# Kernel tuning notes

Hardware: AMD Instinct MI355X
Metric: run time of the kernel (lower is better)

Reference implementation:

```python
import jax, jax.numpy as jnp
import numpy as np

N, E, K, D = 100000, 3200000, 1024, 11


def setup_inputs() -> dict:
    key = jax.random.key(0)
    ks = jax.random.split(key, 11)
    return {
        "x": jax.random.normal(ks[0], (N, D), jnp.float32),
        "edge_index": jax.random.randint(ks[1], (2, E), 0, N, dtype=jnp.int32),
        "ready_idx": jnp.sort(jax.random.randint(ks[2], (K,), 0, N, dtype=jnp.int32)),
        "W1": jax.random.normal(ks[3], (D, 64), jnp.float32) * 0.2,
        "b1": jax.random.normal(ks[4], (64,), jnp.float32) * 0.02,
        "W2": jax.random.normal(ks[5], (75, 1), jnp.float32) * 0.2,
        "b2": jax.random.normal(ks[6], (1,), jnp.float32) * 0.02,
        "Wd": jax.random.normal(ks[7], (64, 1), jnp.float32) * 0.2,
        "bd": jax.random.normal(ks[8], (1,), jnp.float32) * 0.02,
        "Wv": jax.random.normal(ks[9], (64, 1), jnp.float32) * 0.2,
        "bv": jax.random.normal(ks[10], (1,), jnp.float32) * 0.02,
    }


def gcn_conv(x, W, b, src, dst):
    """PyG GCNConv with flow='target_to_source': gather from dst, aggregate at src.
    Symmetric normalization with self-loops (weight 1)."""
    n = x.shape[0]
    h = x @ W  # [N, F_out]
    loop = jnp.arange(n, dtype=src.dtype)
    s = jnp.concatenate([src, loop])  # aggregation index (row for target_to_source)
    d = jnp.concatenate([dst, loop])  # gather index
    deg = jax.ops.segment_sum(jnp.ones(s.shape, h.dtype), s, num_segments=n)
    dis = jnp.where(deg > 0, jax.lax.rsqrt(jnp.maximum(deg, 1e-12)), 0.0)
    norm = dis[s] * dis[d]  # [E+N]
    out = jax.ops.segment_sum(norm[:, None] * h[d], s, num_segments=n)
    return out + b


def reference(x, edge_index, ready_idx, W1, b1, W2, b2, Wd, bd, Wv, bv):
    src, dst = edge_index[0], edge_index[1]
    h = jax.nn.relu(gcn_conv(x, W1, b1, src, dst))           # [N, 64]
    x_input = jnp.concatenate([h, x], axis=1)                # [N, 75]
    probs_n = gcn_conv(x_input, W2, b2, src, dst)            # [N, 1]
    x_mean = jnp.mean(h, axis=0)                             # [64]
    v = x_mean @ Wv + bv                                     # [1]
    prob_nothing = x_mean @ Wd + bd                          # [1]
    logits = jnp.concatenate([probs_n[ready_idx, 0], prob_nothing])  # [K+1]
    probs = jax.nn.softmax(logits)
    return probs, v
```

## Files before the change

kernel.cpp:

```cpp
#include <hip/hip_runtime.h>
#include <hip/hip_fp16.h>
#include <math.h>

#define N_ 100000
#define E_ 3200000
#define K_ 1024
#define D_ 11
#define NBUCK_ 391
#define NPAD_ (NBUCK_ * 256)
#define CAPB_ 16384
#define CAP_ 32
#define CAPW_ 33
#define GB_ 512
#define CHUNK_ 6256
#define SA_ 8
#define SD_ 4
#define XC_ 32
#define RSEG_ 4096
#define RSTRIDE_ 16

static inline size_t align512(size_t x) { return (x + 511) & ~(size_t)511; }

__device__ inline float2 h2f(unsigned int u) {
    __half2 h = *reinterpret_cast<__half2*>(&u);
    return __half22float2(h);
}

__global__ void k_prep(const float* __restrict__ x, const int* __restrict__ ready,
                       __half* __restrict__ xh,
                       int* __restrict__ deg, float* __restrict__ pr_raw,
                       unsigned char* __restrict__ flag, float* __restrict__ xpart,
                       int* __restrict__ bcur, int* __restrict__ rcntp) {
    int i = blockIdx.x * blockDim.x + threadIdx.x;
    if (i < N_ * 16) {
        int n = i >> 4, j = i & 15;
        if (j < D_) xh[i] = __float2half_rn(x[n * D_ + j]);
    }
    if (i < N_) {
        deg[i] = 0; pr_raw[i] = 0.f;
        int lo = 0, hi = K_ - 1, f = 0;
        while (lo <= hi) {
            int mid = (lo + hi) >> 1;
            int v = ready[mid];
            if (v == i) { f = 1; break; }
            if (v < i) lo = mid + 1; else hi = mid - 1;
        }
        flag[i] = (unsigned char)f;
    }
    if (i < XC_ * 64) xpart[i] = 0.f;
    if (i < NBUCK_) bcur[i] = i * CAPB_;
    if (i < 32 * RSTRIDE_) rcntp[i] = 0;
}

__global__ __launch_bounds__(256) void k_bin(const int* __restrict__ src,
                                             const int* __restrict__ dst,
                                             int* __restrict__ bcur,
                                             int* __restrict__ gbuf) {
    __shared__ int sbuf[NBUCK_ * CAPW_];
    __shared__ int scnt[NBUCK_];
    int t = threadIdx.x;
    for (int b = t; b < NBUCK_; b += 256) scnt[b] = 0;
    __syncthreads();
    long e0 = (long)blockIdx.x * CHUNK_;
    for (int r = 0; r < CHUNK_; r += 2048) {
        int off = r + t * 8;
        long i0 = e0 + off;
        if (off < CHUNK_ && i0 + 7 < E_) {
            int4 s0 = *(const int4*)(src + i0);
            int4 s1 = *(const int4*)(src + i0 + 4);
            int4 d0 = *(const int4*)(dst + i0);
            int4 d1 = *(const int4*)(dst + i0 + 4);
            int ss[8] = {s0.x, s0.y, s0.z, s0.w, s1.x, s1.y, s1.z, s1.w};
            int dd[8] = {d0.x, d0.y, d0.z, d0.w, d1.x, d1.y, d1.z, d1.w};
#pragma unroll
            for (int q = 0; q < 8; q++) {
                int b = ss[q] >> 8;
                int pack = ((ss[q] & 255) << 17) | dd[q];
                int pos = atomicAdd(&scnt[b], 1);
                if (pos < CAP_) sbuf[b * CAPW_ + pos] = pack;
                else gbuf[atomicAdd(&bcur[b], 1)] = pack;
            }
        }
    }
    __syncthreads();
    for (int b = t; b < NBUCK_; b += 256) {
        int c = min(scnt[b], CAP_);
        while (c >= 16) {
            int g = atomicAdd(&bcur[b], 16);
            c -= 16;
            if ((g & 3) == 0) {
                int4* gp = (int4*)(gbuf + g);
#pragma unroll
                for (int q = 0; q < 4; q++)
                    gp[q] = make_int4(sbuf[b*CAPW_ + c + 4*q],
                                      sbuf[b*CAPW_ + c + 4*q + 1],
                                      sbuf[b*CAPW_ + c + 4*q + 2],
                                      sbuf[b*CAPW_ + c + 4*q + 3]);
            } else {
                for (int k = 0; k < 16; k++) gbuf[g + k] = sbuf[b*CAPW_ + c + k];
            }
        }
        if (c > 0) {
            int g = atomicAdd(&bcur[b], c);
            for (int k = 0; k < c; k++) gbuf[g + k] = sbuf[b*CAPW_ + k];
        }
    }
}

__global__ __launch_bounds__(256) void k_deg(const int* __restrict__ bcur,
                                             const int* __restrict__ gbuf,
                                             int* __restrict__ deg) {
    __shared__ int hist[256];
    int t = threadIdx.x, b = blockIdx.x, s = blockIdx.y;
    hist[t] = 0;
    __syncthreads();
    int base = b * CAPB_;
    int cnt = min(bcur[b] - base, CAPB_);
    int seg = (((cnt + SD_ - 1) / SD_) + 3) & ~3;
    int lo = s * seg, hi = min(lo + seg, cnt);
    int p = lo + t * 4;
    for (; p + 3 < hi; p += 1024) {
        int4 v = *(const int4*)(gbuf + base + p);
        atomicAdd(&hist[v.x >> 17], 1);
        atomicAdd(&hist[v.y >> 17], 1);
        atomicAdd(&hist[v.z >> 17], 1);
        atomicAdd(&hist[v.w >> 17], 1);
    }
    if (p < hi) {
        for (int q = p; q < hi; q++) atomicAdd(&hist[gbuf[base + q] >> 17], 1);
    }
    __syncthreads();
    int node = (b << 8) + t;
    if (node < N_ && hist[t]) atomicAdd(&deg[node], hist[t]);
}

__global__ void k_dis(const int* __restrict__ deg, float* __restrict__ dis,
                      __half* __restrict__ xh) {
    int i = blockIdx.x * blockDim.x + threadIdx.x;
    if (i >= N_) return;
    float dv = rsqrtf((float)(deg[i] + 1));
    dis[i] = dv;
    xh[(size_t)i * 16 + 11] = __float2half_rn(dv);
}

__global__ __launch_bounds__(256) void k_agg(const int* __restrict__ bcur,
                                             const int* __restrict__ gbuf,
                                             const __half* __restrict__ xh,
                                             const unsigned char* __restrict__ flag,
                                             float* __restrict__ upart,
                                             int* __restrict__ rcntp,
                                             int2* __restrict__ redge) {
    __shared__ int sorted[2048];
    __shared__ int hist[256];
    __shared__ int incl[256];
    __shared__ int offa[256];
    int t = threadIdx.x, b = blockIdx.x, s = blockIdx.y;
    hist[t] = 0;
    __syncthreads();
    int base = b * CAPB_;
    int cnt = min(bcur[b] - base, CAPB_);
    int seg = (cnt + SA_ - 1) / SA_;
    int lo = s * seg, hi = min(lo + seg, cnt);
    int segn = hi - lo;
    int kmax = (segn + 255) >> 8;
    int pk[8], rk[8];
    for (int k = 0; k < kmax; k++) {
        int idx = lo + (k << 8) + t;
        if (idx < hi) {
            pk[k] = gbuf[base + idx];
            rk[k] = atomicAdd(&hist[pk[k] >> 17], 1);
        } else pk[k] = -1;
    }
    __syncthreads();
    incl[t] = hist[t];
    __syncthreads();
    for (int off = 1; off < 256; off <<= 1) {
        int v = (t >= off) ? incl[t - off] : 0;
        __syncthreads();
        incl[t] += v;
        __syncthreads();
    }
    offa[t] = incl[t] - hist[t];
    __syncthreads();
    for (int k = 0; k < kmax; k++) {
        if (pk[k] >= 0) sorted[offa[pk[k] >> 17] + rk[k]] = pk[k];
    }
    __syncthreads();
    int my_start = offa[t], my_cnt = hist[t];
    int node = (b << 8) + t;
    const uint4* xr = (const uint4*)xh;
    float acc[D_];
#pragma unroll
    for (int j = 0; j < D_; j++) acc[j] = 0.f;
    int i = 0;
    for (; i + 3 < my_cnt; i += 4) {
        int pp[4];
#pragma unroll
        for (int q = 0; q < 4; q++) pp[q] = sorted[my_start + i + q];
        uint4 A[4], B[4];
#pragma unroll
        for (int q = 0; q < 4; q++) {
            size_t r = (size_t)(pp[q] & 131071) * 2;
            A[q] = xr[r]; B[q] = xr[r + 1];
        }
#pragma unroll
        for (int q = 0; q < 4; q++) {
            float2 f0 = h2f(A[q].x), f1 = h2f(A[q].y), f2 = h2f(A[q].z);
            float2 f3 = h2f(A[q].w), f4 = h2f(B[q].x), f5 = h2f(B[q].y);
            float w = f5.y;
            acc[0]  = fmaf(w, f0.x, acc[0]);
            acc[1]  = fmaf(w, f0.y, acc[1]);
            acc[2]  = fmaf(w, f1.x, acc[2]);
            acc[3]  = fmaf(w, f1.y, acc[3]);
            acc[4]  = fmaf(w, f2.x, acc[4]);
            acc[5]  = fmaf(w, f2.y, acc[5]);
            acc[6]  = fmaf(w, f3.x, acc[6]);
            acc[7]  = fmaf(w, f3.y, acc[7]);
            acc[8]  = fmaf(w, f4.x, acc[8]);
            acc[9]  = fmaf(w, f4.y, acc[9]);
            acc[10] = fmaf(w, f5.x, acc[10]);
        }
    }
    for (; i < my_cnt; i++) {
        int pack = sorted[my_start + i];
        size_t r = (size_t)(pack & 131071) * 2;
        uint4 A = xr[r], B = xr[r + 1];
        float2 f0 = h2f(A.x), f1 = h2f(A.y), f2 = h2f(A.z);
        float2 f3 = h2f(A.w), f4 = h2f(B.x), f5 = h2f(B.y);
        float w = f5.y;
        acc[0]  = fmaf(w, f0.x, acc[0]);
        acc[1]  = fmaf(w, f0.y, acc[1]);
        acc[2]  = fmaf(w, f1.x, acc[2]);
        acc[3]  = fmaf(w, f1.y, acc[3]);
        acc[4]  = fmaf(w, f2.x, acc[4]);
        acc[5]  = fmaf(w, f2.y, acc[5]);
        acc[6]  = fmaf(w, f3.x, acc[6]);
        acc[7]  = fmaf(w, f3.y, acc[7]);
        acc[8]  = fmaf(w, f4.x, acc[8]);
        acc[9]  = fmaf(w, f4.y, acc[9]);
        acc[10] = fmaf(w, f5.x, acc[10]);
    }
    float* dst = upart + ((size_t)s * NPAD_ + node) * 12;
    ((float4*)dst)[0] = make_float4(acc[0], acc[1], acc[2],  acc[3]);
    ((float4*)dst)[1] = make_float4(acc[4], acc[5], acc[6],  acc[7]);
    ((float4*)dst)[2] = make_float4(acc[8], acc[9], acc[10], 0.f);

    if (node < N_ && my_cnt > 0 && flag[node]) {
        int r = (b * SA_ + s) & 31;
        int slot = atomicAdd(&rcntp[r * RSTRIDE_], my_cnt);
        int lim = min(my_cnt, max(0, RSEG_ - slot));
        for (int i2 = 0; i2 < lim; i2++)
            redge[(r << 12) + slot + i2] =
                make_int2(node, sorted[my_start + i2] & 131071);
    }
}

__global__ __launch_bounds__(256) void k_node(
    const float* __restrict__ upart, const float* __restrict__ x,
    const float* __restrict__ dis,
    const float* __restrict__ W1, const float* __restrict__ b1,
    const float* __restrict__ W2,
    float* __restrict__ hd, float* __restrict__ xpart) {
    __shared__ float sW1[D_ * 64];
    __shared__ float sb1[64];
    __shared__ float sW2[75];
    __shared__ float smean[64];
    int t = threadIdx.x;
    for (int k = t; k < D_ * 64; k += 256) sW1[k] = W1[k];
    if (t < 64) { sb1[t] = b1[t]; smean[t] = 0.f; }
    if (t < 75) sW2[t] = W2[t];
    __syncthreads();

    int nl = t >> 2, q = t & 3;
    int node = blockIdx.x * 64 + nl;
    bool valid = node < N_;

    float4 mine = make_float4(0.f, 0.f, 0.f, 0.f);
    if (valid && q < 3) {
        const int TOT3 = NPAD_ * 3;
        int slot = node * 3 + q;
        const float4* up = (const float4*)upart;
        float4 a = up[slot];
#pragma unroll
        for (int s = 1; s < SA_; s++) {
            float4 v = up[(size_t)s * TOT3 + slot];
            a.x += v.x; a.y += v.y; a.z += v.z; a.w += v.w;
        }
        mine = a;
    }
    int lb = (t & 63) & ~3;
    float acc[D_];
    acc[0]  = __shfl(mine.x, lb);     acc[1]  = __shfl(mine.y, lb);
    acc[2]  = __shfl(mine.z, lb);     acc[3]  = __shfl(mine.w, lb);
    acc[4]  = __shfl(mine.x, lb + 1); acc[5]  = __shfl(mine.y, lb + 1);
    acc[6]  = __shfl(mine.z, lb + 1); acc[7]  = __shfl(mine.w, lb + 1);
    acc[8]  = __shfl(mine.x, lb + 2); acc[9]  = __shfl(mine.y, lb + 2);
    acc[10] = __shfl(mine.z, lb + 2);

    float hreg[16];
    float h2v = 0.f;
    float di = 0.f;
    if (valid) {
        di = dis[node];
        float xr_[D_], g[D_];
#pragma unroll
        for (int j = 0; j < D_; j++) xr_[j] = x[(size_t)node * D_ + j];
#pragma unroll
        for (int j = 0; j < D_; j++) g[j] = di * (acc[j] + di * xr_[j]);

        int fbase = q << 4;
#pragma unroll
        for (int j = 0; j < 16; j++) {
            int f = fbase + j;
            float a = sb1[f];
#pragma unroll
            for (int jj = 0; jj < D_; jj++) a = fmaf(g[jj], sW1[jj * 64 + f], a);
            float hf = fmaxf(a, 0.f);
            hreg[j] = hf;
            h2v = fmaf(hf, sW2[f], h2v);
        }
        if (q == 0) {
#pragma unroll
            for (int jj = 0; jj < D_; jj++) h2v = fmaf(xr_[jj], sW2[64 + jj], h2v);
        }
    } else {
#pragma unroll
        for (int j = 0; j < 16; j++) hreg[j] = 0.f;
    }
    h2v += __shfl_xor(h2v, 1);
    h2v += __shfl_xor(h2v, 2);
    if (valid && q == 0) hd[node] = di * h2v;

    int lane = t & 63;
#pragma unroll
    for (int j = 0; j < 16; j++) {
        float v = hreg[j];
        v += __shfl_xor(v, 4);
        v += __shfl_xor(v, 8);
        v += __shfl_xor(v, 16);
        v += __shfl_xor(v, 32);
        if (lane < 4) atomicAdd(&smean[(lane << 4) + j], v);
    }
    __syncthreads();
    if (t < 64) atomicAdd(&xpart[((blockIdx.x & (XC_ - 1)) << 6) + t], smean[t]);
}

__global__ void k_pr(const int* __restrict__ rcntp, const int2* __restrict__ redge,
                     const float* __restrict__ hd, float* __restrict__ pr_raw) {
    int idx = blockIdx.x * blockDim.x + threadIdx.x;
    int r = idx >> 12;
    int off = idx & (RSEG_ - 1);
    if (r < 32 && off < min(rcntp[r * RSTRIDE_], RSEG_)) {
        int2 e = redge[(r << 12) + off];
        atomicAdd(&pr_raw[e.x], hd[e.y]);
    }
}

__global__ __launch_bounds__(1024) void k_final(
    const int* __restrict__ ready, const float* __restrict__ dis,
    const float* __restrict__ hd, const float* __restrict__ pr_raw,
    const float* __restrict__ xpart,
    const float* __restrict__ b2,
    const float* __restrict__ Wd, const float* __restrict__ bd,
    const float* __restrict__ Wv, const float* __restrict__ bv,
    float* __restrict__ out) {
    __shared__ float xm[64];
    __shared__ float red[1024];
    __shared__ float s_max, s_sum, s_pn, s_v;
    int t = threadIdx.x;
    if (t < 64) {
        float s = 0.f;
#pragma unroll
        for (int c = 0; c < XC_; c++) s += xpart[(c << 6) + t];
        xm[t] = s * (1.0f / N_);
    }
    __syncthreads();
    if (t == 0) {
        float pn = bd[0], vv = bv[0];
        for (int f = 0; f < 64; f++) { pn += xm[f] * Wd[f]; vv += xm[f] * Wv[f]; }
        s_pn = pn; s_v = vv;
    }
    int r = ready[t];
    float dr = dis[r];
    float l = dr * (pr_raw[r] + hd[r]) + b2[0];
    __syncthreads();
    float pn = s_pn;
    red[t] = (t == 0) ? fmaxf(l, pn) : l;
    __syncthreads();
    for (int sft = 512; sft > 0; sft >>= 1) {
        if (t < sft) red[t] = fmaxf(red[t], red[t + sft]);
        __syncthreads();
    }
    if (t == 0) s_max = red[0];
    __syncthreads();
    float m = s_max;
    float el = expf(l - m);
    red[t] = el + ((t == 0) ? expf(pn - m) : 0.f);
    __syncthreads();
    for (int sft = 512; sft > 0; sft >>= 1) {
        if (t < sft) red[t] += red[t + sft];
        __syncthreads();
    }
    if (t == 0) s_sum = red[0];
    __syncthreads();
    float inv = 1.0f / s_sum;
    out[t] = el * inv;
    if (t == 0) {
        out[K_] = expf(pn - m) * inv;
        out[K_ + 1] = s_v;
    }
}

extern "C" void kernel_launch(void* const* d_in, const int* in_sizes, int n_in,
                              void* d_out, int out_size, void* d_ws, size_t ws_size,
                              hipStream_t stream) {
    const float* x    = (const float*)d_in[0];
    const int*   ei   = (const int*)d_in[1];
    const int*   src  = ei;
    const int*   dst  = ei + E_;
    const int*   ready= (const int*)d_in[2];
    const float* W1   = (const float*)d_in[3];
    const float* b1   = (const float*)d_in[4];
    const float* W2   = (const float*)d_in[5];
    const float* b2   = (const float*)d_in[6];
    const float* Wd   = (const float*)d_in[7];
    const float* bd   = (const float*)d_in[8];
    const float* Wv   = (const float*)d_in[9];
    const float* bv   = (const float*)d_in[10];
    float* out = (float*)d_out;

    char* ws = (char*)d_ws;
    size_t o = 0;
    int*   bcur   = (int*)(ws + o);          o += align512(NBUCK_ * sizeof(int));
    int*   rcntp  = (int*)(ws + o);          o += align512(32 * RSTRIDE_ * sizeof(int));
    int*   gbuf   = (int*)(ws + o);          o += align512((size_t)NBUCK_ * CAPB_ * sizeof(int));
    float* upart  = (float*)(ws + o);        o += align512((size_t)SA_ * NPAD_ * 12 * sizeof(float));
    __half* xh    = (__half*)(ws + o);       o += align512((size_t)N_ * 16 * sizeof(__half));
    int2*  redge  = (int2*)(ws + o);         o += align512((size_t)32 * RSEG_ * sizeof(int2));
    int*   deg    = (int*)(ws + o);          o += align512(N_ * sizeof(int));
    float* dis    = (float*)(ws + o);        o += align512(N_ * sizeof(float));
    float* hd     = (float*)(ws + o);        o += align512(N_ * sizeof(float));
    float* pr_raw = (float*)(ws + o);        o += align512(N_ * sizeof(float));
    unsigned char* flag = (unsigned char*)(ws + o); o += align512(N_);
    float* xpart  = (float*)(ws + o);        o += align512(XC_ * 64 * sizeof(float));

    const int B = 256;
    int g_node  = (N_ + B - 1) / B;
    int g_node4 = (N_ + 63) / 64;
    int g_prep  = (N_ * 16 + B - 1) / B;
    int g_pr    = (32 * RSEG_) / B;
    dim3 gdeg(NBUCK_, SD_);
    dim3 gagg(NBUCK_, SA_);

    k_prep <<<g_prep, B, 0, stream>>>(x, ready, xh, deg, pr_raw, flag, xpart, bcur, rcntp);
    k_bin  <<<GB_, B, 0, stream>>>(src, dst, bcur, gbuf);
    k_deg  <<<gdeg, B, 0, stream>>>(bcur, gbuf, deg);
    k_dis  <<<g_node, B, 0, stream>>>(deg, dis, xh);
    k_agg  <<<gagg, B, 0, stream>>>(bcur, gbuf, xh, flag, upart, rcntp, redge);
    k_node <<<g_node4, B, 0, stream>>>(upart, x, dis, W1, b1, W2, hd, xpart);
    k_pr   <<<g_pr, B, 0, stream>>>(rcntp, redge, hd, pr_raw);
    k_final<<<1, 1024, 0, stream>>>(ready, dis, hd, pr_raw, xpart,
                                    b2, Wd, bd, Wv, bv, out);
}
```

Measured before the change: 206.4 us.

## Fuse degree, normalization and aggregation kernels into one cooperative kernel

```diff
diff --git a/kernel.cpp b/kernel.cpp
--- a/kernel.cpp
+++ b/kernel.cpp
@@ -1,6 +1,9 @@
 #include <hip/hip_runtime.h>
+#include <hip/hip_cooperative_groups.h>
 #include <hip/hip_fp16.h>
 #include <math.h>
+
+namespace cg = cooperative_groups;
 
 #define N_ 100000
 #define E_ 3200000
@@ -107,45 +110,11 @@
     }
 }
 
-__global__ __launch_bounds__(256) void k_deg(const int* __restrict__ bcur,
+__global__ __launch_bounds__(256) void k_mid(const int* __restrict__ bcur,
                                              const int* __restrict__ gbuf,
-                                             int* __restrict__ deg) {
-    __shared__ int hist[256];
-    int t = threadIdx.x, b = blockIdx.x, s = blockIdx.y;
-    hist[t] = 0;
-    __syncthreads();
-    int base = b * CAPB_;
-    int cnt = min(bcur[b] - base, CAPB_);
-    int seg = (((cnt + SD_ - 1) / SD_) + 3) & ~3;
-    int lo = s * seg, hi = min(lo + seg, cnt);
-    int p = lo + t * 4;
-    for (; p + 3 < hi; p += 1024) {
-        int4 v = *(const int4*)(gbuf + base + p);
-        atomicAdd(&hist[v.x >> 17], 1);
-        atomicAdd(&hist[v.y >> 17], 1);
-        atomicAdd(&hist[v.z >> 17], 1);
-        atomicAdd(&hist[v.w >> 17], 1);
-    }
-    if (p < hi) {
-        for (int q = p; q < hi; q++) atomicAdd(&hist[gbuf[base + q] >> 17], 1);
-    }
-    __syncthreads();
-    int node = (b << 8) + t;
-    if (node < N_ && hist[t]) atomicAdd(&deg[node], hist[t]);
-}
-
-__global__ void k_dis(const int* __restrict__ deg, float* __restrict__ dis,
-                      __half* __restrict__ xh) {
-    int i = blockIdx.x * blockDim.x + threadIdx.x;
-    if (i >= N_) return;
-    float dv = rsqrtf((float)(deg[i] + 1));
-    dis[i] = dv;
-    xh[(size_t)i * 16 + 11] = __float2half_rn(dv);
-}
-
-__global__ __launch_bounds__(256) void k_agg(const int* __restrict__ bcur,
-                                             const int* __restrict__ gbuf,
-                                             const __half* __restrict__ xh,
+                                             int* __restrict__ deg,
+                                             float* __restrict__ dis,
+                                             __half* __restrict__ xh,
                                              const unsigned char* __restrict__ flag,
                                              float* __restrict__ upart,
                                              int* __restrict__ rcntp,
@@ -154,59 +123,118 @@
     __shared__ int hist[256];
     __shared__ int incl[256];
     __shared__ int offa[256];
-    int t = threadIdx.x, b = blockIdx.x, s = blockIdx.y;
-    hist[t] = 0;
-    __syncthreads();
-    int base = b * CAPB_;
-    int cnt = min(bcur[b] - base, CAPB_);
-    int seg = (cnt + SA_ - 1) / SA_;
-    int lo = s * seg, hi = min(lo + seg, cnt);
-    int segn = hi - lo;
-    int kmax = (segn + 255) >> 8;
-    int pk[8], rk[8];
-    for (int k = 0; k < kmax; k++) {
-        int idx = lo + (k << 8) + t;
-        if (idx < hi) {
-            pk[k] = gbuf[base + idx];
-            rk[k] = atomicAdd(&hist[pk[k] >> 17], 1);
-        } else pk[k] = -1;
-    }
-    __syncthreads();
-    incl[t] = hist[t];
-    __syncthreads();
-    for (int off = 1; off < 256; off <<= 1) {
-        int v = (t >= off) ? incl[t - off] : 0;
-        __syncthreads();
-        incl[t] += v;
-        __syncthreads();
-    }
-    offa[t] = incl[t] - hist[t];
-    __syncthreads();
-    for (int k = 0; k < kmax; k++) {
-        if (pk[k] >= 0) sorted[offa[pk[k] >> 17] + rk[k]] = pk[k];
-    }
-    __syncthreads();
-    int my_start = offa[t], my_cnt = hist[t];
-    int node = (b << 8) + t;
+    cg::grid_group grid = cg::this_grid();
+    int t = threadIdx.x;
+
+    for (int u = blockIdx.x; u < NBUCK_ * SD_; u += gridDim.x) {
+        int b = u >> 2, s = u & (SD_ - 1);
+        hist[t] = 0;
+        __syncthreads();
+        int base = b * CAPB_;
+        int cnt = min(bcur[b] - base, CAPB_);
+        int seg = (((cnt + SD_ - 1) / SD_) + 3) & ~3;
+        int lo = s * seg, hi = min(lo + seg, cnt);
+        int p = lo + t * 4;
+        for (; p + 3 < hi; p += 1024) {
+            int4 v = *(const int4*)(gbuf + base + p);
+            atomicAdd(&hist[v.x >> 17], 1);
+            atomicAdd(&hist[v.y >> 17], 1);
+            atomicAdd(&hist[v.z >> 17], 1);
+            atomicAdd(&hist[v.w >> 17], 1);
+        }
+        if (p < hi) {
+            for (int q = p; q < hi; q++) atomicAdd(&hist[gbuf[base + q] >> 17], 1);
+        }
+        __syncthreads();
+        int node = (b << 8) + t;
+        if (node < N_ && hist[t]) atomicAdd(&deg[node], hist[t]);
+    }
+    grid.sync();
+
+    for (int u = blockIdx.x; u < NBUCK_; u += gridDim.x) {
+        int node = (u << 8) + t;
+        if (node < N_) {
+            float dv = rsqrtf((float)(deg[node] + 1));
+            dis[node] = dv;
+            xh[(size_t)node * 16 + 11] = __float2half_rn(dv);
+        }
+    }
+    grid.sync();
+
     const uint4* xr = (const uint4*)xh;
-    float acc[D_];
-#pragma unroll
-    for (int j = 0; j < D_; j++) acc[j] = 0.f;
-    int i = 0;
-    for (; i + 3 < my_cnt; i += 4) {
-        int pp[4];
-#pragma unroll
-        for (int q = 0; q < 4; q++) pp[q] = sorted[my_start + i + q];
-        uint4 A[4], B[4];
-#pragma unroll
-        for (int q = 0; q < 4; q++) {
-            size_t r = (size_t)(pp[q] & 131071) * 2;
-            A[q] = xr[r]; B[q] = xr[r + 1];
-        }
-#pragma unroll
-        for (int q = 0; q < 4; q++) {
-            float2 f0 = h2f(A[q].x), f1 = h2f(A[q].y), f2 = h2f(A[q].z);
-            float2 f3 = h2f(A[q].w), f4 = h2f(B[q].x), f5 = h2f(B[q].y);
+    for (int u = blockIdx.x; u < NBUCK_ * SA_; u += gridDim.x) {
+        int b = u >> 3, s = u & (SA_ - 1);
+        hist[t] = 0;
+        __syncthreads();
+        int base = b * CAPB_;
+        int cnt = min(bcur[b] - base, CAPB_);
+        int seg = (cnt + SA_ - 1) / SA_;
+        int lo = s * seg, hi = min(lo + seg, cnt);
+        int segn = hi - lo;
+        int kmax = (segn + 255) >> 8;
+        int pk[8], rk[8];
+        for (int k = 0; k < kmax; k++) {
+            int idx = lo + (k << 8) + t;
+            if (idx < hi) {
+                pk[k] = gbuf[base + idx];
+                rk[k] = atomicAdd(&hist[pk[k] >> 17], 1);
+            } else pk[k] = -1;
+        }
+        __syncthreads();
+        incl[t] = hist[t];
+        __syncthreads();
+        for (int off = 1; off < 256; off <<= 1) {
+            int v = (t >= off) ? incl[t - off] : 0;
+            __syncthreads();
+            incl[t] += v;
+            __syncthreads();
+        }
+        offa[t] = incl[t] - hist[t];
+        __syncthreads();
+        for (int k = 0; k < kmax; k++) {
+            if (pk[k] >= 0) sorted[offa[pk[k] >> 17] + rk[k]] = pk[k];
+        }
+        __syncthreads();
+        int my_start = offa[t], my_cnt = hist[t];
+        int node = (b << 8) + t;
+        float acc[D_];
+#pragma unroll
+        for (int j = 0; j < D_; j++) acc[j] = 0.f;
+        int i = 0;
+        for (; i + 3 < my_cnt; i += 4) {
+            int pp[4];
+#pragma unroll
+            for (int q = 0; q < 4; q++) pp[q] = sorted[my_start + i + q];
+            uint4 A[4], B[4];
+#pragma unroll
+            for (int q = 0; q < 4; q++) {
+                size_t r = (size_t)(pp[q] & 131071) * 2;
+                A[q] = xr[r]; B[q] = xr[r + 1];
+            }
+#pragma unroll
+            for (int q = 0; q < 4; q++) {
+                float2 f0 = h2f(A[q].x), f1 = h2f(A[q].y), f2 = h2f(A[q].z);
+                float2 f3 = h2f(A[q].w), f4 = h2f(B[q].x), f5 = h2f(B[q].y);
+                float w = f5.y;
+                acc[0]  = fmaf(w, f0.x, acc[0]);
+                acc[1]  = fmaf(w, f0.y, acc[1]);
+                acc[2]  = fmaf(w, f1.x, acc[2]);
+                acc[3]  = fmaf(w, f1.y, acc[3]);
+                acc[4]  = fmaf(w, f2.x, acc[4]);
+                acc[5]  = fmaf(w, f2.y, acc[5]);
+                acc[6]  = fmaf(w, f3.x, acc[6]);
+                acc[7]  = fmaf(w, f3.y, acc[7]);
+                acc[8]  = fmaf(w, f4.x, acc[8]);
+                acc[9]  = fmaf(w, f4.y, acc[9]);
+                acc[10] = fmaf(w, f5.x, acc[10]);
+            }
+        }
+        for (; i < my_cnt; i++) {
+            int pack = sorted[my_start + i];
+            size_t r = (size_t)(pack & 131071) * 2;
+            uint4 A = xr[r], B = xr[r + 1];
+            float2 f0 = h2f(A.x), f1 = h2f(A.y), f2 = h2f(A.z);
+            float2 f3 = h2f(A.w), f4 = h2f(B.x), f5 = h2f(B.y);
             float w = f5.y;
             acc[0]  = fmaf(w, f0.x, acc[0]);
             acc[1]  = fmaf(w, f0.y, acc[1]);
@@ -220,38 +248,19 @@
             acc[9]  = fmaf(w, f4.y, acc[9]);
             acc[10] = fmaf(w, f5.x, acc[10]);
         }
-    }
-    for (; i < my_cnt; i++) {
-        int pack = sorted[my_start + i];
-        size_t r = (size_t)(pack & 131071) * 2;
-        uint4 A = xr[r], B = xr[r + 1];
-        float2 f0 = h2f(A.x), f1 = h2f(A.y), f2 = h2f(A.z);
-        float2 f3 = h2f(A.w), f4 = h2f(B.x), f5 = h2f(B.y);
-        float w = f5.y;
-        acc[0]  = fmaf(w, f0.x, acc[0]);
-        acc[1]  = fmaf(w, f0.y, acc[1]);
-        acc[2]  = fmaf(w, f1.x, acc[2]);
-        acc[3]  = fmaf(w, f1.y, acc[3]);
-        acc[4]  = fmaf(w, f2.x, acc[4]);
-        acc[5]  = fmaf(w, f2.y, acc[5]);
-        acc[6]  = fmaf(w, f3.x, acc[6]);
-        acc[7]  = fmaf(w, f3.y, acc[7]);
-        acc[8]  = fmaf(w, f4.x, acc[8]);
-        acc[9]  = fmaf(w, f4.y, acc[9]);
-        acc[10] = fmaf(w, f5.x, acc[10]);
-    }
-    float* dst = upart + ((size_t)s * NPAD_ + node) * 12;
-    ((float4*)dst)[0] = make_float4(acc[0], acc[1], acc[2],  acc[3]);
-    ((float4*)dst)[1] = make_float4(acc[4], acc[5], acc[6],  acc[7]);
-    ((float4*)dst)[2] = make_float4(acc[8], acc[9], acc[10], 0.f);
-
-    if (node < N_ && my_cnt > 0 && flag[node]) {
-        int r = (b * SA_ + s) & 31;
-        int slot = atomicAdd(&rcntp[r * RSTRIDE_], my_cnt);
-        int lim = min(my_cnt, max(0, RSEG_ - slot));
-        for (int i2 = 0; i2 < lim; i2++)
-            redge[(r << 12) + slot + i2] =
-                make_int2(node, sorted[my_start + i2] & 131071);
+        float* dst = upart + ((size_t)s * NPAD_ + node) * 12;
+        ((float4*)dst)[0] = make_float4(acc[0], acc[1], acc[2],  acc[3]);
+        ((float4*)dst)[1] = make_float4(acc[4], acc[5], acc[6],  acc[7]);
+        ((float4*)dst)[2] = make_float4(acc[8], acc[9], acc[10], 0.f);
+
+        if (node < N_ && my_cnt > 0 && flag[node]) {
+            int r = (b * SA_ + s) & 31;
+            int slot = atomicAdd(&rcntp[r * RSTRIDE_], my_cnt);
+            int lim = min(my_cnt, max(0, RSEG_ - slot));
+            for (int i2 = 0; i2 < lim; i2++)
+                redge[(r << 12) + slot + i2] =
+                    make_int2(node, sorted[my_start + i2] & 131071);
+        }
     }
 }
 
@@ -445,18 +454,25 @@
     float* xpart  = (float*)(ws + o);        o += align512(XC_ * 64 * sizeof(float));
 
     const int B = 256;
-    int g_node  = (N_ + B - 1) / B;
     int g_node4 = (N_ + 63) / 64;
     int g_prep  = (N_ * 16 + B - 1) / B;
     int g_pr    = (32 * RSEG_) / B;
-    dim3 gdeg(NBUCK_, SD_);
-    dim3 gagg(NBUCK_, SA_);
+
+    int perCU = 0;
+    hipOccupancyMaxActiveBlocksPerMultiprocessor(&perCU, (const void*)k_mid, B, 0);
+    if (perCU < 1) perCU = 1;
+    int gmid = perCU * 256;
+    if (gmid > NBUCK_ * SA_) gmid = NBUCK_ * SA_;
 
     k_prep <<<g_prep, B, 0, stream>>>(x, ready, xh, deg, pr_raw, flag, xpart, bcur, rcntp);
     k_bin  <<<GB_, B, 0, stream>>>(src, dst, bcur, gbuf);
-    k_deg  <<<gdeg, B, 0, stream>>>(bcur, gbuf, deg);
-    k_dis  <<<g_node, B, 0, stream>>>(deg, dis, xh);
-    k_agg  <<<gagg, B, 0, stream>>>(bcur, gbuf, xh, flag, upart, rcntp, redge);
+    {
+        void* args[] = {(void*)&bcur, (void*)&gbuf, (void*)&deg, (void*)&dis,
+                        (void*)&xh, (void*)&flag, (void*)&upart,
+                        (void*)&rcntp, (void*)&redge};
+        hipLaunchCooperativeKernel((const void*)k_mid, dim3(gmid), dim3(B),
+                                   args, 0, stream);
+    }
     k_node <<<g_node4, B, 0, stream>>>(upart, x, dis, W1, b1, W2, hd, xpart);
     k_pr   <<<g_pr, B, 0, stream>>>(rcntp, redge, hd, pr_raw);
     k_final<<<1, 1024, 0, stream>>>(ready, dis, hd, pr_raw, xpart,
```

New measurement: 373.3 us. 1.81x slower.
